# Optimization experiments

Hardware: AMD Instinct MI355X
Metric: run time of the kernel (lower is better)

The kernel has to match this reference:

```python
import jax, jax.numpy as jnp
import numpy as np

HID = 10  # hidden_dim


def conv1x1(x, w, b=None):
    # x: [N,C,H,W], w: [O,C] -> [N,O,H,W]
    y = jnp.einsum('oc,nchw->nohw', w, x)
    if b is not None:
        y = y + b[None, :, None, None]
    return y


def gconv1x1(x, w, b=None):
    # grouped 1x1 conv. x: [N,G*ipg,H,W], w: [G,opg,ipg]
    N, C, H, W = x.shape
    G, opg, ipg = w.shape
    xg = x.reshape(N, G, ipg, H, W)
    y = jnp.einsum('goi,ngihw->ngohw', w, xg).reshape(N, G * opg, H, W)
    if b is not None:
        y = y + b[None, :, None, None]
    return y


def _decomp(h_fea, xf, xh, att_w, att_b, w):
    # Decomposition: spatial attention from (fea, xf, xh), gate xf, project.
    att = jax.nn.sigmoid(conv1x1(jnp.concatenate([h_fea, xf, xh], axis=1), att_w, att_b))
    xfh = jax.nn.relu(conv1x1(xf * att, w))
    return xfh, att


def _comp(parts, xh, att_w, att_b, w):
    # Composition: parts [P,N,HID,H,W]; grouped per-part attention then fuse with xh.
    ca = jax.nn.sigmoid(jnp.einsum('pc,pnchw->pnhw', att_w[:, 0], parts) + att_b[:, None, None, None])
    msg = (parts * ca[:, :, None]).sum(0)  # [N,HID,H,W]
    return jax.nn.relu(conv1x1(jnp.concatenate([xh, msg], axis=1), w))


def _update(xh, m0, m1, m2, gate_w, gate_b, cand_w):
    # conv_Update: gated residual update from summed messages.
    cat = jnp.concatenate([xh, m0 + m1 + m2], axis=1)
    g = jax.nn.sigmoid(conv1x1(cat, gate_w, gate_b))
    cand = jax.nn.relu(conv1x1(cat, cand_w))
    return xh * (1.0 - g) + cand * g


def half_graph(h_fea, xh_u, xh_l, xf, xp, pdp_w1, pdp_w2, att_w, att_b,
               compU_att_w, compU_att_b, compU_w,
               compL_att_w, compL_att_b, compL_w,
               decU_att_w, decU_att_b, decU_w,
               decL_att_w, decL_att_b, decL_w,
               updU_gate_w, updU_gate_b, updU_cand_w,
               updL_gate_w, updL_gate_b, updL_cand_w):
    # Part_Dependency: shared trunk then grouped conv -> (dp_u, dp_l)
    t = jax.nn.relu(conv1x1(jnp.concatenate([h_fea, xh_u, xh_l], axis=1), pdp_w1))
    dp = jax.nn.relu(gconv1x1(t, pdp_w2))
    dp_u, dp_l = dp[:, :HID], dp[:, HID:]
    # grouped sigmoid attention over the two half nodes
    a = jax.nn.sigmoid(gconv1x1(jnp.concatenate([xh_u, xh_l], axis=1), att_w, att_b))
    ag_u, ag_l = a[:, 0:1], a[:, 1:2]
    # upper half node
    xphu = _comp(xp[0:4], xh_u, compU_att_w, compU_att_b, compU_w)
    xlh = dp_l * ag_l + xh_u * ag_u  # Pair_Part_Dependency (lower -> upper)
    xfhu, att_u = _decomp(h_fea, xf, xh_u, decU_att_w, decU_att_b, decU_w)
    xh_u_new = _update(xh_u, xphu, xlh, xfhu, updU_gate_w, updU_gate_b, updU_cand_w)
    # lower half node
    xphl = _comp(xp[4:6], xh_l, compL_att_w, compL_att_b, compL_w)
    xuh = dp_u * ag_u + xh_l * ag_l  # Pair_Part_Dependency (upper -> lower)
    xfhl, att_l = _decomp(h_fea, xf, xh_l, decL_att_w, decL_att_b, decL_w)
    xh_l_new = _update(xh_l, xphl, xuh, xfhl, updL_gate_w, updL_gate_b, updL_cand_w)
    return xh_u_new, xh_l_new, att_u, att_l


def setup_inputs() -> dict:
    key = jax.random.key(0)
    N, C, H, W = 8, 256, 128, 128
    ks = jax.random.split(key, 32)
    s = 0.05
    inp = {
        'h_fea': jax.random.normal(ks[0], (N, C, H, W), jnp.float32),
        'xh_u': jax.random.normal(ks[1], (N, HID, H, W), jnp.float32),
        'xh_l': jax.random.normal(ks[2], (N, HID, H, W), jnp.float32),
        'xf': jax.random.normal(ks[3], (N, HID, H, W), jnp.float32),
        'xp': jax.random.normal(ks[4], (6, N, HID, H, W), jnp.float32),
        'pdp_w1': jax.random.normal(ks[5], (2 * HID, C + 2 * HID), jnp.float32) * s,
        'pdp_w2': jax.random.normal(ks[6], (2, HID, HID), jnp.float32) * s,
        'att_w': jax.random.normal(ks[7], (2, 1, HID), jnp.float32) * s,
        'att_b': jnp.zeros((2,), jnp.float32),
        'compU_att_w': jax.random.normal(ks[8], (4, 1, HID), jnp.float32) * s,
        'compU_att_b': jnp.zeros((4,), jnp.float32),
        'compU_w': jax.random.normal(ks[9], (HID, 2 * HID), jnp.float32) * s,
        'compL_att_w': jax.random.normal(ks[10], (2, 1, HID), jnp.float32) * s,
        'compL_att_b': jnp.zeros((2,), jnp.float32),
        'compL_w': jax.random.normal(ks[11], (HID, 2 * HID), jnp.float32) * s,
        'decU_att_w': jax.random.normal(ks[12], (1, C + 2 * HID), jnp.float32) * s,
        'decU_att_b': jnp.zeros((1,), jnp.float32),
        'decU_w': jax.random.normal(ks[13], (HID, HID), jnp.float32) * s,
        'decL_att_w': jax.random.normal(ks[14], (1, C + 2 * HID), jnp.float32) * s,
        'decL_att_b': jnp.zeros((1,), jnp.float32),
        'decL_w': jax.random.normal(ks[15], (HID, HID), jnp.float32) * s,
        'updU_gate_w': jax.random.normal(ks[16], (HID, 2 * HID), jnp.float32) * s,
        'updU_gate_b': jnp.zeros((HID,), jnp.float32),
        'updU_cand_w': jax.random.normal(ks[17], (HID, 2 * HID), jnp.float32) * s,
        'updL_gate_w': jax.random.normal(ks[18], (HID, 2 * HID), jnp.float32) * s,
        'updL_gate_b': jnp.zeros((HID,), jnp.float32),
        'updL_cand_w': jax.random.normal(ks[19], (HID, 2 * HID), jnp.float32) * s,
    }
    return inp


def reference(h_fea, xh_u, xh_l, xf, xp, pdp_w1, pdp_w2, att_w, att_b,
              compU_att_w, compU_att_b, compU_w,
              compL_att_w, compL_att_b, compL_w,
              decU_att_w, decU_att_b, decU_w,
              decL_att_w, decL_att_b, decL_w,
              updU_gate_w, updU_gate_b, updU_cand_w,
              updL_gate_w, updL_gate_b, updL_cand_w):
    return half_graph(h_fea, xh_u, xh_l, xf, xp, pdp_w1, pdp_w2, att_w, att_b,
                      compU_att_w, compU_att_b, compU_w,
                      compL_att_w, compL_att_b, compL_w,
                      decU_att_w, decU_att_b, decU_w,
                      decL_att_w, decL_att_b, decL_w,
                      updU_gate_w, updU_gate_b, updU_cand_w,
                      updL_gate_w, updL_gate_b, updL_cand_w)
```

## Files before the change

### kernel.cpp

```cpp
#include <hip/hip_runtime.h>
#include <stdint.h>

typedef unsigned short u16;
typedef unsigned int   u32;
typedef short v8s __attribute__((ext_vector_type(8)));
typedef float v4f __attribute__((ext_vector_type(4)));

#define HW   16384
#define NPIX 131072
#define WST  264
#define DST  266

__device__ __forceinline__ float sigm(float x) { return 1.f / (1.f + __expf(-x)); }
__device__ __forceinline__ u16 f2bf(float f) {
    u32 u = __float_as_uint(f);
    return (u16)((u + 0x7fffu + ((u >> 16) & 1u)) >> 16);
}
__device__ __forceinline__ u32 pk2bf(float a, float b) {
    u32 ua = __float_as_uint(a), ub = __float_as_uint(b);
    u32 ra = (ua + 0x7fffu + ((ua >> 16) & 1u)) >> 16;
    u32 rb = (ub + 0x7fffu + ((ub >> 16) & 1u)) & 0xffff0000u;
    return ra | rb;
}

__global__ __launch_bounds__(256) void half_graph_fused(
    const float* __restrict__ hf,  const float* __restrict__ xhu, const float* __restrict__ xhl,
    const float* __restrict__ xfg, const float* __restrict__ xpg,
    const float* __restrict__ pdp_w1, const float* __restrict__ pdp_w2,
    const float* __restrict__ att_w,  const float* __restrict__ att_b,
    const float* __restrict__ cU_aw, const float* __restrict__ cU_ab, const float* __restrict__ cU_w,
    const float* __restrict__ cL_aw, const float* __restrict__ cL_ab, const float* __restrict__ cL_w,
    const float* __restrict__ dU_aw, const float* __restrict__ dU_ab, const float* __restrict__ dU_w,
    const float* __restrict__ dL_aw, const float* __restrict__ dL_ab, const float* __restrict__ dL_w,
    const float* __restrict__ uU_gw, const float* __restrict__ uU_gb, const float* __restrict__ uU_cw,
    const float* __restrict__ uL_gw, const float* __restrict__ uL_gb, const float* __restrict__ uL_cw,
    float* __restrict__ out)
{
    __shared__ u16   Wlds[32 * WST];
    __shared__ float Dlds[22 * DST];

    const int tid = threadIdx.x;
    const int blk = blockIdx.x;
    const int n   = blk >> 6;
    const int hwb = (blk & 63) * 256;

    for (int i = tid; i < 32 * 256; i += 256) {
        int o = i >> 8, c = i & 255;
        float w = 0.f;
        if (o < 20)       w = pdp_w1[o * 276 + c];
        else if (o == 20) w = dU_aw[c];
        else if (o == 21) w = dL_aw[c];
        Wlds[o * WST + c] = f2bf(w);
    }
    __syncthreads();

    const int wv  = tid >> 6;
    const int ln  = tid & 63;
    const int q   = ln >> 4;
    const int col = ln & 15;
    const float* xb = hf + (size_t)n * 256 * HW + hwb + wv * 64 + col;

    v4f acc[2][4];
    #pragma unroll
    for (int mt = 0; mt < 2; ++mt)
        #pragma unroll
        for (int t = 0; t < 4; ++t) acc[mt][t] = (v4f){0.f, 0.f, 0.f, 0.f};

    float xr[2][4][8];
    #define ISSUE(buf, k0)                                                   \
        {   _Pragma("unroll")                                                \
            for (int t = 0; t < 4; ++t) {                                    \
                _Pragma("unroll")                                            \
                for (int j = 0; j < 8; ++j)                                  \
                    xr[buf][t][j] = xb[(size_t)((k0) + q * 8 + j) * HW + t * 16]; \
            } }

    ISSUE(0, 0)
    #pragma unroll
    for (int ks = 0; ks < 8; ++ks) {
        if (ks < 7) ISSUE((ks + 1) & 1, (ks + 1) * 32)
        v8s a0 = *(const v8s*)&Wlds[(col) * WST + ks * 32 + q * 8];
        v8s a1 = *(const v8s*)&Wlds[(16 + col) * WST + ks * 32 + q * 8];
        const int buf = ks & 1;
        #pragma unroll
        for (int t = 0; t < 4; ++t) {
            union { u32 w[4]; v8s v; } bf;
            #pragma unroll
            for (int i = 0; i < 4; ++i)
                bf.w[i] = pk2bf(xr[buf][t][2 * i], xr[buf][t][2 * i + 1]);
            acc[0][t] = __builtin_amdgcn_mfma_f32_16x16x32_bf16(a0, bf.v, acc[0][t], 0, 0, 0);
            acc[1][t] = __builtin_amdgcn_mfma_f32_16x16x32_bf16(a1, bf.v, acc[1][t], 0, 0, 0);
        }
    }
    #undef ISSUE

    #pragma unroll
    for (int mt = 0; mt < 2; ++mt)
        #pragma unroll
        for (int r = 0; r < 4; ++r) {
            int o = mt * 16 + q * 4 + r;
            if (o < 22) {
                #pragma unroll
                for (int t = 0; t < 4; ++t)
                    Dlds[o * DST + wv * 64 + t * 16 + col] = acc[mt][t][r];
            }
        }
    __syncthreads();

    const int p  = blk * 256 + tid;
    const int hw = p & 16383;

    float accT[20];
    #pragma unroll
    for (int o = 0; o < 20; ++o) accT[o] = Dlds[o * DST + tid];
    const float dU = Dlds[20 * DST + tid], dL = Dlds[21 * DST + tid];

    float xu[10], xl[10], xv[10];
    {
        const float* a = xhu + (size_t)n * 10 * HW + hw;
        const float* b = xhl + (size_t)n * 10 * HW + hw;
        const float* c = xfg + (size_t)n * 10 * HW + hw;
        #pragma unroll
        for (int i = 0; i < 10; ++i) xu[i] = a[i * HW];
        #pragma unroll
        for (int i = 0; i < 10; ++i) xl[i] = b[i * HW];
        #pragma unroll
        for (int i = 0; i < 10; ++i) xv[i] = c[i * HW];
    }

    float t[20];
    #pragma unroll
    for (int o = 0; o < 20; ++o) {
        float s = accT[o];
        #pragma unroll
        for (int i = 0; i < 10; ++i) s = fmaf(pdp_w1[o * 276 + 256 + i], xu[i], s);
        #pragma unroll
        for (int i = 0; i < 10; ++i) s = fmaf(pdp_w1[o * 276 + 266 + i], xl[i], s);
        t[o] = fmaxf(s, 0.f);
    }
    float dpv[20];
    #pragma unroll
    for (int g = 0; g < 2; ++g) {
        #pragma unroll
        for (int o = 0; o < 10; ++o) {
            float s = 0.f;
            #pragma unroll
            for (int i = 0; i < 10; ++i)
                s = fmaf(pdp_w2[(g * 10 + o) * 10 + i], t[g * 10 + i], s);
            dpv[g * 10 + o] = fmaxf(s, 0.f);
        }
    }

    float au_s = att_b[0], al_s = att_b[1];
    #pragma unroll
    for (int i = 0; i < 10; ++i) {
        au_s = fmaf(att_w[i], xu[i], au_s);
        al_s = fmaf(att_w[10 + i], xl[i], al_s);
    }
    const float au = sigm(au_s), al = sigm(al_s);

    float su = dU + dU_ab[0];
    float sl = dL + dL_ab[0];
    #pragma unroll
    for (int i = 0; i < 10; ++i) { su = fmaf(dU_aw[256 + i], xv[i], su); sl = fmaf(dL_aw[256 + i], xv[i], sl); }
    #pragma unroll
    for (int i = 0; i < 10; ++i) { su = fmaf(dU_aw[266 + i], xu[i], su); sl = fmaf(dL_aw[266 + i], xl[i], sl); }
    const float attU = sigm(su), attL = sigm(sl);

    float xfhu[10], xfhl[10];
    #pragma unroll
    for (int o = 0; o < 10; ++o) {
        float a = 0.f, b = 0.f;
        #pragma unroll
        for (int i = 0; i < 10; ++i) {
            a = fmaf(dU_w[o * 10 + i], xv[i], a);
            b = fmaf(dL_w[o * 10 + i], xv[i], b);
        }
        xfhu[o] = fmaxf(attU * a, 0.f);
        xfhl[o] = fmaxf(attL * b, 0.f);
    }

    float msgU[10];
    #pragma unroll
    for (int i = 0; i < 10; ++i) msgU[i] = 0.f;
    #pragma unroll
    for (int pp = 0; pp < 4; ++pp) {
        const float* xq = xpg + (size_t)(pp * 8 + n) * 10 * HW + hw;
        float v[10];
        #pragma unroll
        for (int i = 0; i < 10; ++i) v[i] = xq[i * HW];
        float s = cU_ab[pp];
        #pragma unroll
        for (int i = 0; i < 10; ++i) s = fmaf(cU_aw[pp * 10 + i], v[i], s);
        float ca = sigm(s);
        #pragma unroll
        for (int i = 0; i < 10; ++i) msgU[i] = fmaf(ca, v[i], msgU[i]);
    }
    float xphu[10];
    #pragma unroll
    for (int o = 0; o < 10; ++o) {
        float s = 0.f;
        #pragma unroll
        for (int i = 0; i < 10; ++i) s = fmaf(cU_w[o * 20 + i], xu[i], s);
        #pragma unroll
        for (int i = 0; i < 10; ++i) s = fmaf(cU_w[o * 20 + 10 + i], msgU[i], s);
        xphu[o] = fmaxf(s, 0.f);
    }

    float msgL[10];
    #pragma unroll
    for (int i = 0; i < 10; ++i) msgL[i] = 0.f;
    #pragma unroll
    for (int pp = 4; pp < 6; ++pp) {
        const float* xq = xpg + (size_t)(pp * 8 + n) * 10 * HW + hw;
        float v[10];
        #pragma unroll
        for (int i = 0; i < 10; ++i) v[i] = xq[i * HW];
        float s = cL_ab[pp - 4];
        #pragma unroll
        for (int i = 0; i < 10; ++i) s = fmaf(cL_aw[(pp - 4) * 10 + i], v[i], s);
        float ca = sigm(s);
        #pragma unroll
        for (int i = 0; i < 10; ++i) msgL[i] = fmaf(ca, v[i], msgL[i]);
    }
    float xphl[10];
    #pragma unroll
    for (int o = 0; o < 10; ++o) {
        float s = 0.f;
        #pragma unroll
        for (int i = 0; i < 10; ++i) s = fmaf(cL_w[o * 20 + i], xl[i], s);
        #pragma unroll
        for (int i = 0; i < 10; ++i) s = fmaf(cL_w[o * 20 + 10 + i], msgL[i], s);
        xphl[o] = fmaxf(s, 0.f);
    }

    float outU[10], outL[10];
    {
        float m[10];
        #pragma unroll
        for (int i = 0; i < 10; ++i)
            m[i] = xphu[i] + (dpv[10 + i] * al + xu[i] * au) + xfhu[i];
        #pragma unroll
        for (int o = 0; o < 10; ++o) {
            float gs = uU_gb[o], cs = 0.f;
            #pragma unroll
            for (int i = 0; i < 10; ++i) {
                gs = fmaf(uU_gw[o * 20 + i], xu[i], gs);
                cs = fmaf(uU_cw[o * 20 + i], xu[i], cs);
            }
            #pragma unroll
            for (int i = 0; i < 10; ++i) {
                gs = fmaf(uU_gw[o * 20 + 10 + i], m[i], gs);
                cs = fmaf(uU_cw[o * 20 + 10 + i], m[i], cs);
            }
            float g = sigm(gs), cd = fmaxf(cs, 0.f);
            outU[o] = xu[o] * (1.f - g) + cd * g;
        }
    }
    {
        float m[10];
        #pragma unroll
        for (int i = 0; i < 10; ++i)
            m[i] = xphl[i] + (dpv[i] * au + xl[i] * al) + xfhl[i];
        #pragma unroll
        for (int o = 0; o < 10; ++o) {
            float gs = uL_gb[o], cs = 0.f;
            #pragma unroll
            for (int i = 0; i < 10; ++i) {
                gs = fmaf(uL_gw[o * 20 + i], xl[i], gs);
                cs = fmaf(uL_cw[o * 20 + i], xl[i], cs);
            }
            #pragma unroll
            for (int i = 0; i < 10; ++i) {
                gs = fmaf(uL_gw[o * 20 + 10 + i], m[i], gs);
                cs = fmaf(uL_cw[o * 20 + 10 + i], m[i], cs);
            }
            float g = sigm(gs), cd = fmaxf(cs, 0.f);
            outL[o] = xl[o] * (1.f - g) + cd * g;
        }
    }

    {
        int baseU = n * 10 * HW + hw;
        #pragma unroll
        for (int c = 0; c < 10; ++c) out[baseU + c * HW] = outU[c];
        int baseL = 1310720 + baseU;
        #pragma unroll
        for (int c = 0; c < 10; ++c) out[baseL + c * HW] = outL[c];
        out[2621440 + n * HW + hw] = attU;
        out[2752512 + n * HW + hw] = attL;
    }
}

extern "C" void kernel_launch(void* const* d_in, const int* in_sizes, int n_in,
                              void* d_out, int out_size, void* d_ws, size_t ws_size,
                              hipStream_t stream) {
    (void)in_sizes; (void)n_in; (void)out_size; (void)d_ws; (void)ws_size;
    const float* hf   = (const float*)d_in[0];
    const float* xhu  = (const float*)d_in[1];
    const float* xhl  = (const float*)d_in[2];
    const float* xfg  = (const float*)d_in[3];
    const float* xpg  = (const float*)d_in[4];
    const float* w1   = (const float*)d_in[5];
    const float* w2   = (const float*)d_in[6];
    const float* aw   = (const float*)d_in[7];
    const float* ab   = (const float*)d_in[8];
    const float* cUaw = (const float*)d_in[9];
    const float* cUab = (const float*)d_in[10];
    const float* cUw  = (const float*)d_in[11];
    const float* cLaw = (const float*)d_in[12];
    const float* cLab = (const float*)d_in[13];
    const float* cLw  = (const float*)d_in[14];
    const float* dUaw = (const float*)d_in[15];
    const float* dUab = (const float*)d_in[16];
    const float* dUw  = (const float*)d_in[17];
    const float* dLaw = (const float*)d_in[18];
    const float* dLab = (const float*)d_in[19];
    const float* dLw  = (const float*)d_in[20];
    const float* uUgw = (const float*)d_in[21];
    const float* uUgb = (const float*)d_in[22];
    const float* uUcw = (const float*)d_in[23];
    const float* uLgw = (const float*)d_in[24];
    const float* uLgb = (const float*)d_in[25];
    const float* uLcw = (const float*)d_in[26];

    dim3 grid(NPIX / 256), block(256);
    hipLaunchKernelGGL(half_graph_fused, grid, block, 0, stream,
        hf, xhu, xhl, xfg, xpg, w1, w2, aw, ab,
        cUaw, cUab, cUw, cLaw, cLab, cLw,
        dUaw, dUab, dUw, dLaw, dLab, dLw,
        uUgw, uUgb, uUcw, uLgw, uLgb, uLcw,
        (float*)d_out);
}
```

Baseline: 304.5 us.

## Stage h_fea tiles into LDS via global_load_lds instead of register prefetch

Result: no change. 308.4 us (+1.3%).

```diff
diff --git a/kernel.cpp b/kernel.cpp
--- a/kernel.cpp
+++ b/kernel.cpp
@@ -9,7 +9,13 @@
 #define HW   16384
 #define NPIX 131072
 #define WST  264
-#define DST  266
+#define DST  264
+#define WBYTES (32 * WST * 2)
+#define XBYTES (32 * 256 * 4)
+#define SMEM_BYTES (WBYTES + XBYTES)
+
+typedef __attribute__((address_space(3))) u32 as3_u32;
+typedef __attribute__((address_space(1))) const u32 as1_u32;
 
 __device__ __forceinline__ float sigm(float x) { return 1.f / (1.f + __expf(-x)); }
 __device__ __forceinline__ u16 f2bf(float f) {
@@ -23,7 +29,7 @@
     return ra | rb;
 }
 
-__global__ __launch_bounds__(256) void half_graph_fused(
+__global__ __launch_bounds__(256, 3) void half_graph_fused(
     const float* __restrict__ hf,  const float* __restrict__ xhu, const float* __restrict__ xhl,
     const float* __restrict__ xfg, const float* __restrict__ xpg,
     const float* __restrict__ pdp_w1, const float* __restrict__ pdp_w2,
@@ -36,8 +42,10 @@
     const float* __restrict__ uL_gw, const float* __restrict__ uL_gb, const float* __restrict__ uL_cw,
     float* __restrict__ out)
 {
-    __shared__ u16   Wlds[32 * WST];
-    __shared__ float Dlds[22 * DST];
+    extern __shared__ char smem[];
+    u16*   Wlds = (u16*)smem;
+    float* Xbuf = (float*)(smem + WBYTES);
+    float* Dlds = (float*)(smem + WBYTES);
 
     const int tid = threadIdx.x;
     const int blk = blockIdx.x;
@@ -52,13 +60,12 @@
         else if (o == 21) w = dL_aw[c];
         Wlds[o * WST + c] = f2bf(w);
     }
-    __syncthreads();
 
     const int wv  = tid >> 6;
     const int ln  = tid & 63;
     const int q   = ln >> 4;
     const int col = ln & 15;
-    const float* xb = hf + (size_t)n * 256 * HW + hwb + wv * 64 + col;
+    const float* hfbase = hf + (size_t)n * 256 * HW + hwb;
 
     v4f acc[2][4];
     #pragma unroll
@@ -66,33 +73,34 @@
         #pragma unroll
         for (int t = 0; t < 4; ++t) acc[mt][t] = (v4f){0.f, 0.f, 0.f, 0.f};
 
-    float xr[2][4][8];
-    #define ISSUE(buf, k0)                                                   \
-        {   _Pragma("unroll")                                                \
-            for (int t = 0; t < 4; ++t) {                                    \
-                _Pragma("unroll")                                            \
-                for (int j = 0; j < 8; ++j)                                  \
-                    xr[buf][t][j] = xb[(size_t)((k0) + q * 8 + j) * HW + t * 16]; \
-            } }
-
-    ISSUE(0, 0)
-    #pragma unroll
-    for (int ks = 0; ks < 8; ++ks) {
-        if (ks < 7) ISSUE((ks + 1) & 1, (ks + 1) * 32)
-        v8s a0 = *(const v8s*)&Wlds[(col) * WST + ks * 32 + q * 8];
-        v8s a1 = *(const v8s*)&Wlds[(16 + col) * WST + ks * 32 + q * 8];
-        const int buf = ks & 1;
+    for (int kc = 0; kc < 8; ++kc) {
+        __syncthreads();
+        #pragma unroll
+        for (int s = 0; s < 8; ++s) {
+            const int r = wv * 8 + s;
+            const float* gp = hfbase + (size_t)(kc * 32 + r) * HW + ln * 4;
+            __builtin_amdgcn_global_load_lds((as1_u32*)gp,
+                (as3_u32*)&Xbuf[r * 256 + ln * 4], 16, 0, 0);
+        }
+        __syncthreads();
+
+        v8s a0 = *(const v8s*)&Wlds[(col)      * WST + kc * 32 + q * 8];
+        v8s a1 = *(const v8s*)&Wlds[(16 + col) * WST + kc * 32 + q * 8];
         #pragma unroll
         for (int t = 0; t < 4; ++t) {
+            const int px = wv * 64 + t * 16 + col;
             union { u32 w[4]; v8s v; } bf;
             #pragma unroll
-            for (int i = 0; i < 4; ++i)
-                bf.w[i] = pk2bf(xr[buf][t][2 * i], xr[buf][t][2 * i + 1]);
+            for (int i = 0; i < 4; ++i) {
+                float x0 = Xbuf[(q * 8 + 2 * i)     * 256 + px];
+                float x1 = Xbuf[(q * 8 + 2 * i + 1) * 256 + px];
+                bf.w[i] = pk2bf(x0, x1);
+            }
             acc[0][t] = __builtin_amdgcn_mfma_f32_16x16x32_bf16(a0, bf.v, acc[0][t], 0, 0, 0);
             acc[1][t] = __builtin_amdgcn_mfma_f32_16x16x32_bf16(a1, bf.v, acc[1][t], 0, 0, 0);
         }
     }
-    #undef ISSUE
+    __syncthreads();
 
     #pragma unroll
     for (int mt = 0; mt < 2; ++mt)
@@ -325,7 +333,7 @@
     const float* uLcw = (const float*)d_in[26];
 
     dim3 grid(NPIX / 256), block(256);
-    hipLaunchKernelGGL(half_graph_fused, grid, block, 0, stream,
+    hipLaunchKernelGGL(half_graph_fused, grid, block, SMEM_BYTES, stream,
         hf, xhu, xhl, xfg, xpg, w1, w2, aw, ab,
         cUaw, cUab, cUw, cLaw, cLab, cLw,
         dUaw, dUab, dUw, dLaw, dLab, dLw,
```
